# Optimization experiments

Measured on AMD Instinct MI355X. Metric: run time of the kernel, lower is better.

## Reference

```python
import jax, jax.numpy as jnp
import numpy as np

N_NODES = 100_000
N_EDGES = 1_000_000
VOCAB = 10_000
HID = 75
OUT = 64
BN_EPS = 1e-5


def gcn_conv(x, edge_index, W, b, n):
    # PyG GCNConv: add self-loops, symmetric deg^{-1/2} normalization, then scatter-add.
    loop = jnp.arange(n, dtype=edge_index.dtype)
    src = jnp.concatenate([edge_index[0], loop])
    dst = jnp.concatenate([edge_index[1], loop])
    deg = jax.ops.segment_sum(jnp.ones_like(src, dtype=x.dtype), dst, num_segments=n)
    dinv = jnp.where(deg > 0, jax.lax.rsqrt(deg), 0.0)
    norm = dinv[src] * dinv[dst]              # [E+N]
    h = x @ W                                  # linear before propagate (PyG order)
    msg = h[src] * norm[:, None]               # gather + per-edge scale
    out = jax.ops.segment_sum(msg, dst, num_segments=n)
    return out + b


def batch_norm(x, gamma, beta):
    # BatchNorm1d over nodes, training mode (biased variance)
    mu = jnp.mean(x, axis=0)
    var = jnp.mean(jnp.square(x - mu), axis=0)
    return (x - mu) * jax.lax.rsqrt(var + BN_EPS) * gamma + beta


def setup_inputs() -> dict:
    key = jax.random.key(0)
    ks = jax.random.split(key, 8)
    x = jax.random.randint(ks[0], (N_NODES,), 0, VOCAB, dtype=jnp.int64)
    edge_index = jax.random.randint(ks[1], (2, N_EDGES), 0, N_NODES, dtype=jnp.int64)
    emb = jax.random.normal(ks[2], (VOCAB, HID), dtype=jnp.float32)
    scale = 1.0 / np.sqrt(HID)
    Ws = jax.random.normal(ks[3], (4, HID, HID), dtype=jnp.float32) * scale
    bs = jnp.zeros((4, HID), dtype=jnp.float32)
    gammas = jnp.ones((4, HID), dtype=jnp.float32)
    betas = jnp.zeros((4, HID), dtype=jnp.float32)
    W_mu = jax.random.normal(ks[4], (HID, OUT), dtype=jnp.float32) * scale
    b_mu = jnp.zeros((OUT,), dtype=jnp.float32)
    W_logstd = jax.random.normal(ks[5], (HID, OUT), dtype=jnp.float32) * scale
    b_logstd = jnp.zeros((OUT,), dtype=jnp.float32)
    return {"x": x, "edge_index": edge_index, "emb": emb, "Ws": Ws, "bs": bs,
            "gammas": gammas, "betas": betas, "W_mu": W_mu, "b_mu": b_mu,
            "W_logstd": W_logstd, "b_logstd": b_logstd}


def reference(x, edge_index, emb, Ws, bs, gammas, betas, W_mu, b_mu, W_logstd, b_logstd):
    h = emb[x]  # [N, 75] embedding lookup
    for i in range(4):
        h = jax.nn.relu(batch_norm(gcn_conv(h, edge_index, Ws[i], bs[i], N_NODES), gammas[i], betas[i]))
    mu = gcn_conv(h, edge_index, W_mu, b_mu, N_NODES)
    logstd = gcn_conv(h, edge_index, W_logstd, b_logstd, N_NODES)
    return (mu, logstd)
```

## Files before the change

kernel.cpp:

```cpp
#include <hip/hip_runtime.h>

#define NN 100000
#define NE 1000000
#define HID 75
#define SP 80
#define OUTF 64
#define BN_EPS 1e-5f

#define SCAN_ELEMS 1024
#define SCAN_NBLK ((NN + SCAN_ELEMS - 1) / SCAN_ELEMS)

__device__ __forceinline__ ushort f2bf(float f) {
    unsigned u = __float_as_uint(f);
    u += 0x7FFF + ((u >> 16) & 1);
    return (ushort)(u >> 16);
}
__device__ __forceinline__ float bf_lo(unsigned u) { return __uint_as_float(u << 16); }
__device__ __forceinline__ float bf_hi(unsigned u) { return __uint_as_float(u & 0xFFFF0000u); }

__global__ void hist_kernel(const int* __restrict__ dst, int* __restrict__ hist, int E) {
    int e = blockIdx.x * blockDim.x + threadIdx.x;
    if (e < E) atomicAdd(&hist[dst[e]], 1);
}

__global__ void dinv_kernel(const int* __restrict__ hist, float* __restrict__ dinv, int n) {
    int i = blockIdx.x * blockDim.x + threadIdx.x;
    if (i < n) dinv[i] = rsqrtf((float)hist[i] + 1.0f);
}

__global__ void scan_pass1(const int* __restrict__ hist, int* __restrict__ bsum) {
    __shared__ int sdata[256];
    int base = blockIdx.x * SCAN_ELEMS;
    int t = threadIdx.x;
    int s = 0;
    #pragma unroll
    for (int k = 0; k < 4; ++k) {
        int i = base + t * 4 + k;
        if (i < NN) s += hist[i];
    }
    sdata[t] = s;
    __syncthreads();
    for (int off = 128; off > 0; off >>= 1) {
        if (t < off) sdata[t] += sdata[t + off];
        __syncthreads();
    }
    if (t == 0) bsum[blockIdx.x] = sdata[0];
}

__global__ void scan_pass2(int* __restrict__ bsum, int* __restrict__ row_ptr, int nblk) {
    if (threadIdx.x == 0) {
        int acc = 0;
        for (int i = 0; i < nblk; ++i) { int v = bsum[i]; bsum[i] = acc; acc += v; }
        row_ptr[NN] = acc;
    }
}

__global__ void scan_pass3(const int* __restrict__ hist, const int* __restrict__ bsum,
                           int* __restrict__ row_ptr) {
    __shared__ int sdata[256];
    int base = blockIdx.x * SCAN_ELEMS;
    int t = threadIdx.x;
    int v[4];
    int s = 0;
    #pragma unroll
    for (int k = 0; k < 4; ++k) {
        int i = base + t * 4 + k;
        v[k] = (i < NN) ? hist[i] : 0;
        s += v[k];
    }
    sdata[t] = s;
    __syncthreads();
    for (int off = 1; off < 256; off <<= 1) {
        int x = (t >= off) ? sdata[t - off] : 0;
        __syncthreads();
        sdata[t] += x;
        __syncthreads();
    }
    int pre = bsum[blockIdx.x] + sdata[t] - s;
    #pragma unroll
    for (int k = 0; k < 4; ++k) {
        int i = base + t * 4 + k;
        if (i < NN) { row_ptr[i] = pre; pre += v[k]; }
    }
}

__global__ void csr_fill(const int* __restrict__ src, const int* __restrict__ dst,
                         const int* __restrict__ row_ptr, int* __restrict__ cnt,
                         int* __restrict__ col, int E) {
    int e = blockIdx.x * blockDim.x + threadIdx.x;
    if (e >= E) return;
    int d = dst[e];
    int slot = row_ptr[d] + atomicAdd(&cnt[d], 1);
    col[slot] = src[e];
}

__global__ void embed_kernel(const int* __restrict__ x, const float* __restrict__ emb,
                             float* __restrict__ h) {
    int t = blockIdx.x * blockDim.x + threadIdx.x;
    if (t >= NN * SP) return;
    int node = t / SP, f = t % SP;
    h[t] = (f < HID) ? emb[x[node] * HID + f] : 0.0f;
}

template<int J, bool BNRELU>
__global__ __launch_bounds__(256, 4)
void gemm_kernel(const float* __restrict__ h, const float* __restrict__ W,
                 const float* __restrict__ ab, const float* __restrict__ dinv,
                 ushort* __restrict__ outb) {
    constexpr int CJ = (J + 3) / 4;
    constexpr int JP = CJ * 4;
    constexpr int NB = 256 / CJ;
    constexpr int RPT = 2;
    constexpr int ROWS = NB * RPT;
    constexpr int OS = (J == HID) ? 80 : 64;
    __shared__ __align__(16) float Wlds[76 * JP];
    __shared__ __align__(16) float sA[SP];
    __shared__ __align__(16) float sC[SP];
    int tl = threadIdx.x;
    for (int idx = tl; idx < 76 * JP; idx += 256) {
        int k = idx / JP, j = idx % JP;
        Wlds[idx] = (k < HID && j < J) ? W[k * J + j] : 0.0f;
    }
    if (BNRELU && tl < SP) { sA[tl] = ab[tl]; sC[tl] = ab[SP + tl]; }
    __syncthreads();
    int nn_local = tl / CJ;
    int c = tl % CJ;
    if (nn_local >= NB) return;
    int r0 = blockIdx.x * ROWS + nn_local * RPT;
    if (r0 >= NN) return;
    int r1 = min(r0 + 1, NN - 1);
    const float* h0 = h + (size_t)r0 * SP;
    const float* h1 = h + (size_t)r1 * SP;
    const float* wbase = Wlds + c * 4;
    float4 acc0 = make_float4(0.f, 0.f, 0.f, 0.f);
    float4 acc1 = make_float4(0.f, 0.f, 0.f, 0.f);
    #pragma unroll 2
    for (int k4 = 0; k4 < 19; ++k4) {
        const float* wr = wbase + (k4 * 4) * JP;
        float4 w0 = *reinterpret_cast<const float4*>(wr);
        float4 w1 = *reinterpret_cast<const float4*>(wr + JP);
        float4 w2 = *reinterpret_cast<const float4*>(wr + 2 * JP);
        float4 w3 = *reinterpret_cast<const float4*>(wr + 3 * JP);
        float4 x0 = *reinterpret_cast<const float4*>(h0 + k4 * 4);
        float4 x1 = *reinterpret_cast<const float4*>(h1 + k4 * 4);
        if (BNRELU) {
            float4 a4 = *reinterpret_cast<const float4*>(sA + k4 * 4);
            float4 c4 = *reinterpret_cast<const float4*>(sC + k4 * 4);
            x0.x = fmaxf(fmaf(x0.x, a4.x, c4.x), 0.f);
            x0.y = fmaxf(fmaf(x0.y, a4.y, c4.y), 0.f);
            x0.z = fmaxf(fmaf(x0.z, a4.z, c4.z), 0.f);
            x0.w = fmaxf(fmaf(x0.w, a4.w, c4.w), 0.f);
            x1.x = fmaxf(fmaf(x1.x, a4.x, c4.x), 0.f);
            x1.y = fmaxf(fmaf(x1.y, a4.y, c4.y), 0.f);
            x1.z = fmaxf(fmaf(x1.z, a4.z, c4.z), 0.f);
            x1.w = fmaxf(fmaf(x1.w, a4.w, c4.w), 0.f);
        }
        acc0.x = fmaf(x0.x, w0.x, acc0.x); acc0.y = fmaf(x0.x, w0.y, acc0.y);
        acc0.z = fmaf(x0.x, w0.z, acc0.z); acc0.w = fmaf(x0.x, w0.w, acc0.w);
        acc0.x = fmaf(x0.y, w1.x, acc0.x); acc0.y = fmaf(x0.y, w1.y, acc0.y);
        acc0.z = fmaf(x0.y, w1.z, acc0.z); acc0.w = fmaf(x0.y, w1.w, acc0.w);
        acc0.x = fmaf(x0.z, w2.x, acc0.x); acc0.y = fmaf(x0.z, w2.y, acc0.y);
        acc0.z = fmaf(x0.z, w2.z, acc0.z); acc0.w = fmaf(x0.z, w2.w, acc0.w);
        acc0.x = fmaf(x0.w, w3.x, acc0.x); acc0.y = fmaf(x0.w, w3.y, acc0.y);
        acc0.z = fmaf(x0.w, w3.z, acc0.z); acc0.w = fmaf(x0.w, w3.w, acc0.w);
        acc1.x = fmaf(x1.x, w0.x, acc1.x); acc1.y = fmaf(x1.x, w0.y, acc1.y);
        acc1.z = fmaf(x1.x, w0.z, acc1.z); acc1.w = fmaf(x1.x, w0.w, acc1.w);
        acc1.x = fmaf(x1.y, w1.x, acc1.x); acc1.y = fmaf(x1.y, w1.y, acc1.y);
        acc1.z = fmaf(x1.y, w1.z, acc1.z); acc1.w = fmaf(x1.y, w1.w, acc1.w);
        acc1.x = fmaf(x1.z, w2.x, acc1.x); acc1.y = fmaf(x1.z, w2.y, acc1.y);
        acc1.z = fmaf(x1.z, w2.z, acc1.z); acc1.w = fmaf(x1.z, w2.w, acc1.w);
        acc1.x = fmaf(x1.w, w3.x, acc1.x); acc1.y = fmaf(x1.w, w3.y, acc1.y);
        acc1.z = fmaf(x1.w, w3.z, acc1.z); acc1.w = fmaf(x1.w, w3.w, acc1.w);
    }
    float d0 = dinv[r0];
    ushort4 o;
    ushort* orow = outb + (size_t)r0 * OS;
    o.x = f2bf(acc0.x * d0); o.y = f2bf(acc0.y * d0); o.z = f2bf(acc0.z * d0); o.w = f2bf(acc0.w * d0);
    reinterpret_cast<ushort4*>(orow)[c] = o;
    if (J == HID && c == 0) reinterpret_cast<ushort4*>(orow)[19] = make_ushort4(0, 0, 0, 0);
    if (r0 + 1 < NN) {
        float d1 = dinv[r1];
        orow = outb + (size_t)r1 * OS;
        o.x = f2bf(acc1.x * d1); o.y = f2bf(acc1.y * d1); o.z = f2bf(acc1.z * d1); o.w = f2bf(acc1.w * d1);
        reinterpret_cast<ushort4*>(orow)[c] = o;
        if (J == HID && c == 0) reinterpret_cast<ushort4*>(orow)[19] = make_ushort4(0, 0, 0, 0);
    }
}

#define ACCUM(W) \
    a0 += bf_lo(W.x); a1 += bf_hi(W.x); a2 += bf_lo(W.y); a3 += bf_hi(W.y);

__global__ void gather75(const int* __restrict__ row_ptr, const int* __restrict__ col,
                         const uint2* __restrict__ hWb, const float* __restrict__ dinv,
                         float* __restrict__ agg) {
    int t = blockIdx.x * 256 + threadIdx.x;
    if (t >= NN * 20) return;
    int n = t / 20, c = t % 20;
    int beg = row_ptr[n], end = row_ptr[n + 1];
    uint2 v = hWb[(size_t)n * 20 + c];
    float a0 = bf_lo(v.x), a1 = bf_hi(v.x), a2 = bf_lo(v.y), a3 = bf_hi(v.y);
    int e = beg;
    for (; e + 3 < end; e += 4) {
        int s0 = col[e], s1 = col[e + 1], s2 = col[e + 2], s3 = col[e + 3];
        uint2 w0 = hWb[(size_t)s0 * 20 + c];
        uint2 w1 = hWb[(size_t)s1 * 20 + c];
        uint2 w2 = hWb[(size_t)s2 * 20 + c];
        uint2 w3 = hWb[(size_t)s3 * 20 + c];
        ACCUM(w0) ACCUM(w1) ACCUM(w2) ACCUM(w3)
    }
    for (; e < end; ++e) {
        uint2 w0 = hWb[(size_t)col[e] * 20 + c];
        ACCUM(w0)
    }
    float d = dinv[n];
    reinterpret_cast<float4*>(agg)[(size_t)n * 20 + c] =
        make_float4(a0 * d, a1 * d, a2 * d, a3 * d);
}

__global__ void gather64(const int* __restrict__ row_ptr, const int* __restrict__ col,
                         const uint2* __restrict__ hWb, const float* __restrict__ dinv,
                         const float* __restrict__ bias, float* __restrict__ out) {
    int t = blockIdx.x * 256 + threadIdx.x;
    int n = t / 16, c = t % 16;
    int beg = row_ptr[n], end = row_ptr[n + 1];
    uint2 v = hWb[(size_t)n * 16 + c];
    float a0 = bf_lo(v.x), a1 = bf_hi(v.x), a2 = bf_lo(v.y), a3 = bf_hi(v.y);
    int e = beg;
    for (; e + 3 < end; e += 4) {
        int s0 = col[e], s1 = col[e + 1], s2 = col[e + 2], s3 = col[e + 3];
        uint2 w0 = hWb[(size_t)s0 * 16 + c];
        uint2 w1 = hWb[(size_t)s1 * 16 + c];
        uint2 w2 = hWb[(size_t)s2 * 16 + c];
        uint2 w3 = hWb[(size_t)s3 * 16 + c];
        ACCUM(w0) ACCUM(w1) ACCUM(w2) ACCUM(w3)
    }
    for (; e < end; ++e) {
        uint2 w0 = hWb[(size_t)col[e] * 16 + c];
        ACCUM(w0)
    }
    float d = dinv[n];
    float4 b = *reinterpret_cast<const float4*>(bias + c * 4);
    reinterpret_cast<float4*>(out)[(size_t)n * 16 + c] =
        make_float4(fmaf(a0, d, b.x), fmaf(a1, d, b.y), fmaf(a2, d, b.z), fmaf(a3, d, b.w));
}

__global__ void stats_kernel(const float* __restrict__ agg, float* __restrict__ stats) {
    __shared__ float ssum[SP], ssq[SP];
    if (threadIdx.x < SP) { ssum[threadIdx.x] = 0.f; ssq[threadIdx.x] = 0.f; }
    __syncthreads();
    int gtid = blockIdx.x * blockDim.x + threadIdx.x;
    int T = gridDim.x * blockDim.x;
    int c = gtid % 20;
    int r = gtid / 20;
    int rstep = T / 20;
    float4 s = make_float4(0.f, 0.f, 0.f, 0.f), q = make_float4(0.f, 0.f, 0.f, 0.f);
    for (; r < NN; r += rstep) {
        float4 v = reinterpret_cast<const float4*>(agg)[r * 20 + c];
        s.x += v.x; s.y += v.y; s.z += v.z; s.w += v.w;
        q.x += v.x * v.x; q.y += v.y * v.y; q.z += v.z * v.z; q.w += v.w * v.w;
    }
    atomicAdd(&ssum[c * 4 + 0], s.x); atomicAdd(&ssum[c * 4 + 1], s.y);
    atomicAdd(&ssum[c * 4 + 2], s.z); atomicAdd(&ssum[c * 4 + 3], s.w);
    atomicAdd(&ssq[c * 4 + 0], q.x); atomicAdd(&ssq[c * 4 + 1], q.y);
    atomicAdd(&ssq[c * 4 + 2], q.z); atomicAdd(&ssq[c * 4 + 3], q.w);
    __syncthreads();
    if (threadIdx.x < SP) {
        atomicAdd(&stats[threadIdx.x], ssum[threadIdx.x]);
        atomicAdd(&stats[SP + threadIdx.x], ssq[threadIdx.x]);
    }
}

__global__ void bn_finalize(const float* __restrict__ stats, const float* __restrict__ gamma,
                            const float* __restrict__ beta, float* __restrict__ ab) {
    int f = threadIdx.x;
    if (f >= SP) return;
    float a = 0.f, cc = 0.f;
    if (f < HID) {
        float mu = stats[f] * (1.0f / NN);
        float var = stats[SP + f] * (1.0f / NN) - mu * mu;
        a = gamma[f] * rsqrtf(var + BN_EPS);
        cc = beta[f] - mu * a;
    }
    ab[f] = a;
    ab[SP + f] = cc;
}

extern "C" void kernel_launch(void* const* d_in, const int* in_sizes, int n_in,
                              void* d_out, int out_size, void* d_ws, size_t ws_size,
                              hipStream_t stream) {
    const int*   x      = (const int*)d_in[0];
    const int*   ei     = (const int*)d_in[1];
    const float* emb    = (const float*)d_in[2];
    const float* Ws     = (const float*)d_in[3];
    const float* gammas = (const float*)d_in[5];
    const float* betas  = (const float*)d_in[6];
    const float* W_mu   = (const float*)d_in[7];
    const float* b_mu   = (const float*)d_in[8];
    const float* W_ls   = (const float*)d_in[9];
    const float* b_ls   = (const float*)d_in[10];
    float* out = (float*)d_out;

    const int E = in_sizes[1] / 2;
    const int* src = ei;
    const int* dst = ei + E;

    char* ws = (char*)d_ws;
    float*  dinv    = (float*) (ws + 0);
    float*  stats   = (float*) (ws + 400000);
    float*  ab      = (float*) (ws + 400640);
    int*    hist    = (int*)   (ws + 401408);
    int*    row_ptr = (int*)   (ws + 801408);
    int*    cnt     = (int*)   (ws + 1201536);
    int*    bsum    = (int*)   (ws + 1601536);
    int*    col     = (int*)   (ws + 1602048);
    float*  hA      = (float*) (ws + 5602048);
    ushort* hBb     = (ushort*)(ws + 37602048);

    hipMemsetAsync(hist, 0, NN * sizeof(int), stream);
    hist_kernel<<<(E + 255) / 256, 256, 0, stream>>>(dst, hist, E);
    dinv_kernel<<<(NN + 255) / 256, 256, 0, stream>>>(hist, dinv, NN);
    scan_pass1<<<SCAN_NBLK, 256, 0, stream>>>(hist, bsum);
    scan_pass2<<<1, 64, 0, stream>>>(bsum, row_ptr, SCAN_NBLK);
    scan_pass3<<<SCAN_NBLK, 256, 0, stream>>>(hist, bsum, row_ptr);
    hipMemsetAsync(cnt, 0, NN * sizeof(int), stream);
    csr_fill<<<(E + 255) / 256, 256, 0, stream>>>(src, dst, row_ptr, cnt, col, E);

    embed_kernel<<<(NN * SP + 255) / 256, 256, 0, stream>>>(x, emb, hA);

    for (int layer = 0; layer < 4; ++layer) {
        const float* W = Ws + (size_t)layer * HID * HID;
        if (layer == 0)
            gemm_kernel<HID, false><<<(NN + 25) / 26, 256, 0, stream>>>(hA, W, ab, dinv, hBb);
        else
            gemm_kernel<HID, true><<<(NN + 25) / 26, 256, 0, stream>>>(hA, W, ab, dinv, hBb);
        gather75<<<(NN * 20 + 255) / 256, 256, 0, stream>>>(row_ptr, col, (const uint2*)hBb, dinv, hA);
        hipMemsetAsync(stats, 0, 2 * SP * sizeof(float), stream);
        stats_kernel<<<640, 256, 0, stream>>>(hA, stats);
        bn_finalize<<<1, 128, 0, stream>>>(stats, gammas + layer * HID, betas + layer * HID, ab);
    }

    gemm_kernel<OUTF, true><<<(NN + 31) / 32, 256, 0, stream>>>(hA, W_mu, ab, dinv, hBb);
    gather64<<<(NN * 16) / 256, 256, 0, stream>>>(row_ptr, col, (const uint2*)hBb, dinv, b_mu, out);

    float* out2 = out + (size_t)NN * OUTF;
    gemm_kernel<OUTF, true><<<(NN + 31) / 32, 256, 0, stream>>>(hA, W_ls, ab, dinv, hBb);
    gather64<<<(NN * 16) / 256, 256, 0, stream>>>(row_ptr, col, (const uint2*)hBb, dinv, b_ls, out2);
}
```

Before: 704.9 us.

## Replace scalar FP32 dense transform with bf16 MFMA matrix-core kernel

Replaces the per-thread FMA GEMM with a kernel that stages a 64-row tile of activations and the weight matrix into shared memory as bf16. It then computes the product with 16x16x32 bf16 MFMA instructions. BN+ReLU and the dinv scaling are still folded into the load and store. The aim is to move the dense transform onto matrix cores and cut VALU work. The cost is lower input precision and scattered 2-byte output stores.

```diff
diff --git a/kernel.cpp b/kernel.cpp
--- a/kernel.cpp
+++ b/kernel.cpp
@@ -6,9 +6,13 @@
 #define SP 80
 #define OUTF 64
 #define BN_EPS 1e-5f
+#define KP 104
 
 #define SCAN_ELEMS 1024
 #define SCAN_NBLK ((NN + SCAN_ELEMS - 1) / SCAN_ELEMS)
+
+typedef short bf16x8 __attribute__((ext_vector_type(8)));
+typedef float f32x4  __attribute__((ext_vector_type(4)));
 
 __device__ __forceinline__ ushort f2bf(float f) {
     unsigned u = __float_as_uint(f);
@@ -103,87 +107,69 @@
 }
 
 template<int J, bool BNRELU>
-__global__ __launch_bounds__(256, 4)
-void gemm_kernel(const float* __restrict__ h, const float* __restrict__ W,
-                 const float* __restrict__ ab, const float* __restrict__ dinv,
-                 ushort* __restrict__ outb) {
-    constexpr int CJ = (J + 3) / 4;
-    constexpr int JP = CJ * 4;
-    constexpr int NB = 256 / CJ;
-    constexpr int RPT = 2;
-    constexpr int ROWS = NB * RPT;
-    constexpr int OS = (J == HID) ? 80 : 64;
-    __shared__ __align__(16) float Wlds[76 * JP];
-    __shared__ __align__(16) float sA[SP];
-    __shared__ __align__(16) float sC[SP];
+__global__ __launch_bounds__(256, 2)
+void gemm_mfma(const float* __restrict__ h, const float* __restrict__ W,
+               const float* __restrict__ ab, const float* __restrict__ dinv,
+               ushort* __restrict__ outb) {
+    constexpr int NT = (J + 15) / 16;
+    constexpr int JP = NT * 16;
+    constexpr int OS = JP;
+    __shared__ ushort Wl[JP * KP];
+    __shared__ ushort Hl[64 * KP];
     int tl = threadIdx.x;
-    for (int idx = tl; idx < 76 * JP; idx += 256) {
-        int k = idx / JP, j = idx % JP;
-        Wlds[idx] = (k < HID && j < J) ? W[k * J + j] : 0.0f;
-    }
-    if (BNRELU && tl < SP) { sA[tl] = ab[tl]; sC[tl] = ab[SP + tl]; }
-    __syncthreads();
-    int nn_local = tl / CJ;
-    int c = tl % CJ;
-    if (nn_local >= NB) return;
-    int r0 = blockIdx.x * ROWS + nn_local * RPT;
-    if (r0 >= NN) return;
-    int r1 = min(r0 + 1, NN - 1);
-    const float* h0 = h + (size_t)r0 * SP;
-    const float* h1 = h + (size_t)r1 * SP;
-    const float* wbase = Wlds + c * 4;
-    float4 acc0 = make_float4(0.f, 0.f, 0.f, 0.f);
-    float4 acc1 = make_float4(0.f, 0.f, 0.f, 0.f);
-    #pragma unroll 2
-    for (int k4 = 0; k4 < 19; ++k4) {
-        const float* wr = wbase + (k4 * 4) * JP;
-        float4 w0 = *reinterpret_cast<const float4*>(wr);
-        float4 w1 = *reinterpret_cast<const float4*>(wr + JP);
-        float4 w2 = *reinterpret_cast<const float4*>(wr + 2 * JP);
-        float4 w3 = *reinterpret_cast<const float4*>(wr + 3 * JP);
-        float4 x0 = *reinterpret_cast<const float4*>(h0 + k4 * 4);
-        float4 x1 = *reinterpret_cast<const float4*>(h1 + k4 * 4);
+    int rbase = blockIdx.x * 64;
+    for (int idx = tl; idx < 96 * JP; idx += 256) {
+        int k = idx / JP, n = idx % JP;
+        float v = (k < HID && n < J) ? W[k * J + n] : 0.0f;
+        Wl[n * KP + k] = f2bf(v);
+    }
+    for (int idx = tl; idx < 64 * 20; idx += 256) {
+        int r = idx / 20, c = idx % 20;
+        int row = rbase + r; if (row >= NN) row = NN - 1;
+        float4 v = reinterpret_cast<const float4*>(h + (size_t)row * SP)[c];
         if (BNRELU) {
-            float4 a4 = *reinterpret_cast<const float4*>(sA + k4 * 4);
-            float4 c4 = *reinterpret_cast<const float4*>(sC + k4 * 4);
-            x0.x = fmaxf(fmaf(x0.x, a4.x, c4.x), 0.f);
-            x0.y = fmaxf(fmaf(x0.y, a4.y, c4.y), 0.f);
-            x0.z = fmaxf(fmaf(x0.z, a4.z, c4.z), 0.f);
-            x0.w = fmaxf(fmaf(x0.w, a4.w, c4.w), 0.f);
-            x1.x = fmaxf(fmaf(x1.x, a4.x, c4.x), 0.f);
-            x1.y = fmaxf(fmaf(x1.y, a4.y, c4.y), 0.f);
-            x1.z = fmaxf(fmaf(x1.z, a4.z, c4.z), 0.f);
-            x1.w = fmaxf(fmaf(x1.w, a4.w, c4.w), 0.f);
+            float4 a4 = reinterpret_cast<const float4*>(ab)[c];
+            float4 c4 = reinterpret_cast<const float4*>(ab + SP)[c];
+            v.x = fmaxf(fmaf(v.x, a4.x, c4.x), 0.f);
+            v.y = fmaxf(fmaf(v.y, a4.y, c4.y), 0.f);
+            v.z = fmaxf(fmaf(v.z, a4.z, c4.z), 0.f);
+            v.w = fmaxf(fmaf(v.w, a4.w, c4.w), 0.f);
         }
-        acc0.x = fmaf(x0.x, w0.x, acc0.x); acc0.y = fmaf(x0.x, w0.y, acc0.y);
-        acc0.z = fmaf(x0.x, w0.z, acc0.z); acc0.w = fmaf(x0.x, w0.w, acc0.w);
-        acc0.x = fmaf(x0.y, w1.x, acc0.x); acc0.y = fmaf(x0.y, w1.y, acc0.y);
-        acc0.z = fmaf(x0.y, w1.z, acc0.z); acc0.w = fmaf(x0.y, w1.w, acc0.w);
-        acc0.x = fmaf(x0.z, w2.x, acc0.x); acc0.y = fmaf(x0.z, w2.y, acc0.y);
-        acc0.z = fmaf(x0.z, w2.z, acc0.z); acc0.w = fmaf(x0.z, w2.w, acc0.w);
-        acc0.x = fmaf(x0.w, w3.x, acc0.x); acc0.y = fmaf(x0.w, w3.y, acc0.y);
-        acc0.z = fmaf(x0.w, w3.z, acc0.z); acc0.w = fmaf(x0.w, w3.w, acc0.w);
-        acc1.x = fmaf(x1.x, w0.x, acc1.x); acc1.y = fmaf(x1.x, w0.y, acc1.y);
-        acc1.z = fmaf(x1.x, w0.z, acc1.z); acc1.w = fmaf(x1.x, w0.w, acc1.w);
-        acc1.x = fmaf(x1.y, w1.x, acc1.x); acc1.y = fmaf(x1.y, w1.y, acc1.y);
-        acc1.z = fmaf(x1.y, w1.z, acc1.z); acc1.w = fmaf(x1.y, w1.w, acc1.w);
-        acc1.x = fmaf(x1.z, w2.x, acc1.x); acc1.y = fmaf(x1.z, w2.y, acc1.y);
-        acc1.z = fmaf(x1.z, w2.z, acc1.z); acc1.w = fmaf(x1.z, w2.w, acc1.w);
-        acc1.x = fmaf(x1.w, w3.x, acc1.x); acc1.y = fmaf(x1.w, w3.y, acc1.y);
-        acc1.z = fmaf(x1.w, w3.z, acc1.z); acc1.w = fmaf(x1.w, w3.w, acc1.w);
-    }
-    float d0 = dinv[r0];
-    ushort4 o;
-    ushort* orow = outb + (size_t)r0 * OS;
-    o.x = f2bf(acc0.x * d0); o.y = f2bf(acc0.y * d0); o.z = f2bf(acc0.z * d0); o.w = f2bf(acc0.w * d0);
-    reinterpret_cast<ushort4*>(orow)[c] = o;
-    if (J == HID && c == 0) reinterpret_cast<ushort4*>(orow)[19] = make_ushort4(0, 0, 0, 0);
-    if (r0 + 1 < NN) {
-        float d1 = dinv[r1];
-        orow = outb + (size_t)r1 * OS;
-        o.x = f2bf(acc1.x * d1); o.y = f2bf(acc1.y * d1); o.z = f2bf(acc1.z * d1); o.w = f2bf(acc1.w * d1);
-        reinterpret_cast<ushort4*>(orow)[c] = o;
-        if (J == HID && c == 0) reinterpret_cast<ushort4*>(orow)[19] = make_ushort4(0, 0, 0, 0);
+        ushort4 u;
+        u.x = f2bf(v.x); u.y = f2bf(v.y); u.z = f2bf(v.z); u.w = f2bf(v.w);
+        *reinterpret_cast<ushort4*>(&Hl[r * KP + c * 4]) = u;
+    }
+    for (int idx = tl; idx < 64 * 16; idx += 256) {
+        int r = idx / 16, k = 80 + (idx % 16);
+        Hl[r * KP + k] = 0;
+    }
+    __syncthreads();
+    int w = tl >> 6;
+    int l = tl & 63;
+    int cq = l & 15;
+    int q  = l >> 4;
+    f32x4 acc[NT] = {};
+    #pragma unroll
+    for (int ks = 0; ks < 3; ++ks) {
+        int k0 = ks * 32 + q * 8;
+        bf16x8 a = *reinterpret_cast<const bf16x8*>(&Hl[(w * 16 + cq) * KP + k0]);
+        #pragma unroll
+        for (int t = 0; t < NT; ++t) {
+            bf16x8 b = *reinterpret_cast<const bf16x8*>(&Wl[(t * 16 + cq) * KP + k0]);
+            acc[t] = __builtin_amdgcn_mfma_f32_16x16x32_bf16(a, b, acc[t], 0, 0, 0);
+        }
+    }
+    int r0 = rbase + w * 16 + q * 4;
+    #pragma unroll
+    for (int r = 0; r < 4; ++r) {
+        int grow = r0 + r;
+        if (grow < NN) {
+            float d = dinv[grow];
+            ushort* orow = outb + (size_t)grow * OS;
+            #pragma unroll
+            for (int t = 0; t < NT; ++t)
+                orow[t * 16 + cq] = f2bf(acc[t][r] * d);
+        }
     }
 }
 
@@ -330,19 +316,19 @@
     for (int layer = 0; layer < 4; ++layer) {
         const float* W = Ws + (size_t)layer * HID * HID;
         if (layer == 0)
-            gemm_kernel<HID, false><<<(NN + 25) / 26, 256, 0, stream>>>(hA, W, ab, dinv, hBb);
+            gemm_mfma<HID, false><<<(NN + 63) / 64, 256, 0, stream>>>(hA, W, ab, dinv, hBb);
         else
-            gemm_kernel<HID, true><<<(NN + 25) / 26, 256, 0, stream>>>(hA, W, ab, dinv, hBb);
+            gemm_mfma<HID, true><<<(NN + 63) / 64, 256, 0, stream>>>(hA, W, ab, dinv, hBb);
         gather75<<<(NN * 20 + 255) / 256, 256, 0, stream>>>(row_ptr, col, (const uint2*)hBb, dinv, hA);
         hipMemsetAsync(stats, 0, 2 * SP * sizeof(float), stream);
         stats_kernel<<<640, 256, 0, stream>>>(hA, stats);
         bn_finalize<<<1, 128, 0, stream>>>(stats, gammas + layer * HID, betas + layer * HID, ab);
     }
 
-    gemm_kernel<OUTF, true><<<(NN + 31) / 32, 256, 0, stream>>>(hA, W_mu, ab, dinv, hBb);
+    gemm_mfma<OUTF, true><<<(NN + 63) / 64, 256, 0, stream>>>(hA, W_mu, ab, dinv, hBb);
     gather64<<<(NN * 16) / 256, 256, 0, stream>>>(row_ptr, col, (const uint2*)hBb, dinv, b_mu, out);
 
     float* out2 = out + (size_t)NN * OUTF;
-    gemm_kernel<OUTF, true><<<(NN + 31) / 32, 256, 0, stream>>>(hA, W_ls, ab, dinv, hBb);
+    gemm_mfma<OUTF, true><<<(NN + 63) / 64, 256, 0, stream>>>(hA, W_ls, ab, dinv, hBb);
     gather64<<<(NN * 16) / 256, 256, 0, stream>>>(row_ptr, col, (const uint2*)hBb, dinv, b_ls, out2);
 }
```

Result: faster. 628.7 us (-10.8%).
